# Performance work log

Measured on AMD Instinct MI355X. Metric: run time of the kernel, lower is better.

## Reference

```python
import jax, jax.numpy as jnp
import numpy as np

B, S, C, P, M, H = 64, 512, 862, 96, 512, 128  # batch, seq_len, enc_in, pred_len, mem_num, hid_size


def setup_inputs() -> dict:
    key = jax.random.key(0)
    ks = jax.random.split(key, 8)
    x = jax.random.normal(ks[0], (B, S, C), dtype=jnp.float32)
    # nn.Linear default init scale ~ 1/sqrt(fan_in)
    W1 = jax.random.normal(ks[1], (H, S), dtype=jnp.float32) / np.float32(np.sqrt(S))
    b1 = jnp.zeros((H,), dtype=jnp.float32)
    Wp = jax.random.normal(ks[2], (H, H), dtype=jnp.float32) / np.float32(np.sqrt(H))
    bp = jnp.zeros((H,), dtype=jnp.float32)
    W2 = jax.random.normal(ks[3], (P, 2 * H), dtype=jnp.float32) / np.float32(np.sqrt(2 * H))
    b2 = jnp.zeros((P,), dtype=jnp.float32)
    # xavier_normal_ with relu gain: std = sqrt(2) * sqrt(2/(fan_in+fan_out))
    mem_std = np.float32(np.sqrt(2.0) * np.sqrt(2.0 / (M + H)))
    memory = jax.random.normal(ks[4], (M, H), dtype=jnp.float32) * mem_std
    return dict(x=x, W1=W1, b1=b1, Wp=Wp, bp=bp, W2=W2, b2=b2, memory=memory)


def reference(x, W1, b1, Wp, bp, W2, b2, memory):
    b, s, c = x.shape
    # get_repre: Linear1 over seq dim, sigmoid, projector
    r = jax.nn.sigmoid(jnp.einsum('bsc,hs->bch', x, W1) + b1)   # [B, C, H]
    r = jnp.einsum('bch,gh->bcg', r, Wp) + bp                    # [B, C, H]
    r = r.reshape(-1, H)                                         # [N, H], N = B*C
    # memory_enhance: codebook attention (topk/distance loss does not affect output)
    att = jax.nn.softmax(jnp.einsum('nd,fd->nf', r, memory), axis=1)  # [N, M]
    out = jnp.einsum('nf,fd->nd', att, memory)                        # [N, H]
    rep = jnp.concatenate([out, r], axis=1).reshape(b, c, 2 * H)      # [B, C, 2H]
    # predict: Linear2 then permute to [B, pred_len, C]
    res = jnp.einsum('bcd,pd->bcp', rep, W2) + b2
    return jnp.transpose(res, (0, 2, 1))
```

## Files before the change

kernel.cpp:

```cpp
#include <hip/hip_runtime.h>
#include <hip/hip_bf16.h>

typedef __attribute__((ext_vector_type(4))) float f32x4;
typedef __attribute__((ext_vector_type(8))) short s16x8;

#define DEVI __device__ __forceinline__

constexpr int S = 512, C = 862, P = 96, H = 128, BATCH = 64;

DEVI short f2bf(float f) {
  unsigned u = __builtin_bit_cast(unsigned, f);
  u += 0x7fffu + ((u >> 16) & 1u);
  return (short)(u >> 16);
}

DEVI unsigned pk2(float a, float b) {
  return (unsigned)(unsigned short)f2bf(a) | ((unsigned)(unsigned short)f2bf(b) << 16);
}

DEVI s16x8 mk8(const float* v) {
  s16x8 r;
#pragma unroll
  for (int i = 0; i < 8; ++i) r[i] = f2bf(v[i]);
  return r;
}

DEVI void gload16(const void* g, void* l) {
  __builtin_amdgcn_global_load_lds(
      (const __attribute__((address_space(1))) void*)g,
      (__attribute__((address_space(3))) void*)l, 16, 0, 0);
}

template <int NK>
DEVI void redistN(const unsigned* p01, const unsigned* p23, int sA, int hi,
                  s16x8* f) {
#pragma unroll
  for (int kc = 0; kc < NK; ++kc) {
    unsigned a0 = __shfl(p01[2 * kc], sA),      b0 = __shfl(p01[2 * kc + 1], sA);
    unsigned a1 = __shfl(p23[2 * kc], sA),      b1 = __shfl(p23[2 * kc + 1], sA);
    unsigned a2 = __shfl(p01[2 * kc], sA + 16), b2 = __shfl(p01[2 * kc + 1], sA + 16);
    unsigned a3 = __shfl(p23[2 * kc], sA + 16), b3 = __shfl(p23[2 * kc + 1], sA + 16);
    union { s16x8 v; unsigned u[4]; } t;
    t.u[0] = hi ? b0 : a0;
    t.u[1] = hi ? b1 : a1;
    t.u[2] = hi ? b2 : a2;
    t.u[3] = hi ? b3 : a3;
    f[kc] = t.v;
  }
}

__global__ __launch_bounds__(256) void k0_convert(
    const float* __restrict__ W1, const float* __restrict__ Wp,
    const float* __restrict__ W2, const float* __restrict__ mem,
    short* __restrict__ W1b, short* __restrict__ WpS, short* __restrict__ W2b,
    short* __restrict__ membS, short* __restrict__ memTS) {
  int i = blockIdx.x * 256 + threadIdx.x;
  if (i < 65536) { W1b[i] = f2bf(W1[i]); return; }
  i -= 65536;
  if (i < 16384) {
    int g = i >> 7, h = i & 127;
    WpS[(g << 7) + (h ^ ((g & 7) << 3))] = f2bf(Wp[i]);
    return;
  }
  i -= 16384;
  if (i < 24576) { W2b[i] = f2bf(W2[i]); return; }
  i -= 24576;
  if (i < 65536) {
    int f = i >> 7, d = i & 127;
    short v = f2bf(mem[i]);
    membS[((f >> 6) << 13) + ((f & 63) << 7) + (d ^ ((f & 7) << 3))] = v;
    memTS[((f >> 6) << 13) + (d << 6) + ((f & 63) ^ ((d & 7) << 3))] = v;
  }
}

__global__ __launch_bounds__(512, 4) void k1_repre(
    const float* __restrict__ x, const short* __restrict__ W1b,
    const float* __restrict__ b1, short* __restrict__ R1b) {
  __shared__ short xt[2][64 * 64];
  __shared__ short w1t[2][128 * 64];
  const int b = blockIdx.y;
  const int c0 = blockIdx.x * 64;
  const int tid = threadIdx.x;
  const int l = tid & 63, w = tid >> 6;
  const int l15 = l & 15, l4 = l >> 4;
  const int csub = (w >> 2) * 32, hsub = (w & 3) * 32;

  f32x4 acc[2][2];
#pragma unroll
  for (int ct = 0; ct < 2; ++ct)
#pragma unroll
    for (int ht = 0; ht < 2; ++ht) acc[ct][ht] = (f32x4){0.f, 0.f, 0.f, 0.f};

  const int cme = tid & 63;
  const int oct = tid >> 6;
  const bool cv = (c0 + cme) < C;
  const float* xsrc0 = x + (size_t)b * S * C + c0 + cme;
  const int hh = tid >> 2, qq = tid & 3;

  float xv[8];
  s16x8 wv[2];
  {
    const float* src = xsrc0 + (size_t)(oct * 8) * C;
#pragma unroll
    for (int i = 0; i < 8; ++i) xv[i] = cv ? src[(size_t)i * C] : 0.f;
    const short* wsrc = W1b + hh * 512;
    wv[0] = *(const s16x8*)&wsrc[qq * 8];
    wv[1] = *(const s16x8*)&wsrc[(qq + 4) * 8];
  }

  for (int kt = 0; kt < 8; ++kt) {
    const int pb = kt & 1;
    *(s16x8*)&xt[pb][cme * 64 + (oct ^ (cme & 7)) * 8] = mk8(xv);
    *(s16x8*)&w1t[pb][hh * 64 + (qq ^ (hh & 7)) * 8] = wv[0];
    *(s16x8*)&w1t[pb][hh * 64 + ((qq + 4) ^ (hh & 7)) * 8] = wv[1];
    __syncthreads();
    if (kt < 7) {
      int kn = kt + 1;
      const float* src = xsrc0 + (size_t)(kn * 64 + oct * 8) * C;
#pragma unroll
      for (int i = 0; i < 8; ++i) xv[i] = cv ? src[(size_t)i * C] : 0.f;
      const short* wsrc = W1b + hh * 512 + kn * 64;
      wv[0] = *(const s16x8*)&wsrc[qq * 8];
      wv[1] = *(const s16x8*)&wsrc[(qq + 4) * 8];
    }
    s16x8 af[2][2], bf[2][2];
#pragma unroll
    for (int ct = 0; ct < 2; ++ct)
#pragma unroll
      for (int kc = 0; kc < 2; ++kc) {
        int row = csub + ct * 16 + l15;
        int slot = kc * 4 + l4;
        af[ct][kc] = *(const s16x8*)&xt[pb][row * 64 + (slot ^ (row & 7)) * 8];
      }
#pragma unroll
    for (int ht = 0; ht < 2; ++ht)
#pragma unroll
      for (int kc = 0; kc < 2; ++kc) {
        int row = hsub + ht * 16 + l15;
        int slot = kc * 4 + l4;
        bf[ht][kc] = *(const s16x8*)&w1t[pb][row * 64 + (slot ^ (row & 7)) * 8];
      }
#pragma unroll
    for (int ct = 0; ct < 2; ++ct)
#pragma unroll
      for (int ht = 0; ht < 2; ++ht)
#pragma unroll
        for (int kc = 0; kc < 2; ++kc)
          acc[ct][ht] = __builtin_amdgcn_mfma_f32_16x16x32_bf16(
              af[ct][kc], bf[ht][kc], acc[ct][ht], 0, 0, 0);
  }
#pragma unroll
  for (int ct = 0; ct < 2; ++ct) {
#pragma unroll
    for (int ht = 0; ht < 2; ++ht) {
      int hcol = hsub + ht * 16 + l15;
      float bias = b1[hcol];
#pragma unroll
      for (int e = 0; e < 4; ++e) {
        int crow = csub + ct * 16 + l4 * 4 + e;
        if (c0 + crow < C) {
          float v = acc[ct][ht][e] + bias;
          float sg = 1.f / (1.f + __expf(-v));
          R1b[((size_t)b * C + c0 + crow) * 128 + hcol] = f2bf(sg);
        }
      }
    }
  }
}

__global__ __launch_bounds__(512, 2) void k2_fused(
    const short* __restrict__ R1b, const short* __restrict__ WpS,
    const float* __restrict__ bp, const short* __restrict__ membS,
    const short* __restrict__ memTS, const short* __restrict__ W2b,
    const float* __restrict__ b2, float* __restrict__ out) {
  __shared__ __align__(16) char lds[65536];
  float* resf = (float*)lds;

  const int b = blockIdx.y, c0 = blockIdx.x * 128;
  const int valid = (C - c0 < 128) ? (C - c0) : 128;
  const int tid = threadIdx.x, l = tid & 63, w = tid >> 6;
  const int l15 = l & 15, l4 = l >> 4;
  const int sA = l15 + 32 * (l4 & 1);
  const int hi = (l4 >> 1) & 1;
  const int xr = (l15 & 7) << 4;
  const int cb = l4 * 16;
  const size_t n0 = (size_t)b * C + c0;

  const int rloc = 16 * w + l15;
  const int rr = rloc < valid ? rloc : valid - 1;

  {
    const char* gwp = (const char*)WpS;
    const char* gmb = (const char*)membS;
    const char* gmt = (const char*)memTS;
#pragma unroll
    for (int i = 0; i < 4; ++i) {
      int o = (w * 4 + i) * 1024;
      gload16(gwp + o + l * 16, lds + 32768 + o);
    }
#pragma unroll
    for (int i = 0; i < 2; ++i) {
      int o = (w * 2 + i) * 1024;
      gload16(gmb + o + l * 16, lds + o);
      gload16(gmt + o + l * 16, lds + 16384 + o);
    }
  }

  s16x8 rb[4];
  {
    const short* r1row = R1b + (n0 + rr) * 128;
#pragma unroll
    for (int kc = 0; kc < 4; ++kc)
      rb[kc] = *(const s16x8*)&r1row[kc * 32 + l4 * 8];
  }
  __syncthreads();

  unsigned rpk01[8], rpk23[8];
  {
    const char* bufWp = lds + 32768;
#pragma unroll
    for (int gt = 0; gt < 8; ++gt) {
      f32x4 acc = (f32x4){0.f, 0.f, 0.f, 0.f};
#pragma unroll
      for (int kc = 0; kc < 4; ++kc) {
        s16x8 af = *(const s16x8*)(bufWp + (gt * 16 + l15) * 256 + ((kc * 64 + cb) ^ xr));
        acc = __builtin_amdgcn_mfma_f32_16x16x32_bf16(af, rb[kc], acc, 0, 0, 0);
      }
      f32x4 bq = *(const f32x4*)&bp[gt * 16 + l4 * 4];
      rpk01[gt] = pk2(acc[0] + bq[0], acc[1] + bq[1]);
      rpk23[gt] = pk2(acc[2] + bq[2], acc[3] + bq[3]);
    }
  }
  s16x8 r2f[4];
  redistN<4>(rpk01, rpk23, sA, hi, r2f);
  __syncthreads();

  float m_run = -1e30f, s_run = 0.f;
  f32x4 oacc[8];
#pragma unroll
  for (int dt = 0; dt < 8; ++dt) oacc[dt] = (f32x4){0.f, 0.f, 0.f, 0.f};

  for (int s = 0; s < 8; ++s) {
    char* bufp = lds + ((s & 1) << 15);
    if (s < 7) {
      char* bufn = lds + (((s + 1) & 1) << 15);
      const char* gmb = (const char*)membS + (size_t)(s + 1) * 16384;
      const char* gmt = (const char*)memTS + (size_t)(s + 1) * 16384;
#pragma unroll
      for (int i = 0; i < 2; ++i) {
        int o = (w * 2 + i) * 1024;
        gload16(gmb + o + l * 16, bufn + o);
        gload16(gmt + o + l * 16, bufn + 16384 + o);
      }
    }
    f32x4 lg[4];
#pragma unroll
    for (int ft = 0; ft < 4; ++ft) {
      lg[ft] = (f32x4){0.f, 0.f, 0.f, 0.f};
#pragma unroll
      for (int kc = 0; kc < 4; ++kc) {
        s16x8 af = *(const s16x8*)(bufp + (ft * 16 + l15) * 256 + ((kc * 64 + cb) ^ xr));
        lg[ft] = __builtin_amdgcn_mfma_f32_16x16x32_bf16(af, r2f[kc], lg[ft], 0, 0, 0);
      }
    }
    float mx = lg[0][0];
#pragma unroll
    for (int ft = 0; ft < 4; ++ft)
#pragma unroll
      for (int e = 0; e < 4; ++e) mx = fmaxf(mx, lg[ft][e]);
    mx = fmaxf(mx, __shfl_xor(mx, 16));
    mx = fmaxf(mx, __shfl_xor(mx, 32));
    float mn = fmaxf(m_run, mx);
    float sc = __expf(m_run - mn);
    float ps = 0.f;
#pragma unroll
    for (int ft = 0; ft < 4; ++ft)
#pragma unroll
      for (int e = 0; e < 4; ++e) {
        float p = __expf(lg[ft][e] - mn);
        lg[ft][e] = p;
        ps += p;
      }
    ps += __shfl_xor(ps, 16);
    ps += __shfl_xor(ps, 32);
    s_run = s_run * sc + ps;
    m_run = mn;
#pragma unroll
    for (int dt = 0; dt < 8; ++dt)
#pragma unroll
      for (int e = 0; e < 4; ++e) oacc[dt][e] *= sc;
    unsigned ppk01[4], ppk23[4];
#pragma unroll
    for (int ft = 0; ft < 4; ++ft) {
      ppk01[ft] = pk2(lg[ft][0], lg[ft][1]);
      ppk23[ft] = pk2(lg[ft][2], lg[ft][3]);
    }
    s16x8 pf[2];
    redistN<2>(ppk01, ppk23, sA, hi, pf);
#pragma unroll
    for (int dt = 0; dt < 8; ++dt) {
#pragma unroll
      for (int kc = 0; kc < 2; ++kc) {
        s16x8 af = *(const s16x8*)(bufp + 16384 + (dt * 16 + l15) * 128 + ((kc * 64 + cb) ^ xr));
        oacc[dt] = __builtin_amdgcn_mfma_f32_16x16x32_bf16(af, pf[kc], oacc[dt], 0, 0, 0);
      }
    }
    __syncthreads();
  }

  s16x8 of[4];
  {
    float inv = 1.f / s_run;
    unsigned opk01[8], opk23[8];
#pragma unroll
    for (int dt = 0; dt < 8; ++dt) {
      opk01[dt] = pk2(oacc[dt][0] * inv, oacc[dt][1] * inv);
      opk23[dt] = pk2(oacc[dt][2] * inv, oacc[dt][3] * inv);
    }
    redistN<4>(opk01, opk23, sA, hi, of);
  }

#pragma unroll
  for (int pt = 0; pt < 6; ++pt) {
    f32x4 acc = (f32x4){0.f, 0.f, 0.f, 0.f};
#pragma unroll
    for (int kc = 0; kc < 4; ++kc) {
      s16x8 af = *(const s16x8*)&W2b[(pt * 16 + l15) * 256 + kc * 32 + l4 * 8];
      acc = __builtin_amdgcn_mfma_f32_16x16x32_bf16(af, of[kc], acc, 0, 0, 0);
    }
#pragma unroll
    for (int kc = 0; kc < 4; ++kc) {
      s16x8 af = *(const s16x8*)&W2b[(pt * 16 + l15) * 256 + 128 + kc * 32 + l4 * 8];
      acc = __builtin_amdgcn_mfma_f32_16x16x32_bf16(af, r2f[kc], acc, 0, 0, 0);
    }
    f32x4 bq = *(const f32x4*)&b2[pt * 16 + l4 * 4];
#pragma unroll
    for (int e = 0; e < 4; ++e)
      resf[rloc * 97 + pt * 16 + l4 * 4 + e] = acc[e] + bq[e];
  }
  __syncthreads();
  {
    int c = tid & 127, p0 = tid >> 7;
    if (c < valid) {
      float* dst = out + (size_t)b * P * C + c0 + c;
#pragma unroll
      for (int j = 0; j < 24; ++j) {
        int p = p0 + j * 4;
        dst[(size_t)p * C] = resf[c * 97 + p];
      }
    }
  }
}

extern "C" void kernel_launch(void* const* d_in, const int* in_sizes, int n_in,
                              void* d_out, int out_size, void* d_ws, size_t ws_size,
                              hipStream_t stream) {
  const float* x   = (const float*)d_in[0];
  const float* W1  = (const float*)d_in[1];
  const float* b1  = (const float*)d_in[2];
  const float* Wp  = (const float*)d_in[3];
  const float* bpv = (const float*)d_in[4];
  const float* W2  = (const float*)d_in[5];
  const float* b2  = (const float*)d_in[6];
  const float* mem = (const float*)d_in[7];
  char* ws = (char*)d_ws;
  short* W1b   = (short*)(ws);
  short* WpS   = (short*)(ws + 131072);
  short* W2b   = (short*)(ws + 163840);
  short* membS = (short*)(ws + 212992);
  short* memTS = (short*)(ws + 344064);
  short* R1b   = (short*)(ws + 475136);
  float* outp = (float*)d_out;

  k0_convert<<<672, 256, 0, stream>>>(W1, Wp, W2, mem, W1b, WpS, W2b, membS, memTS);
  dim3 grid1(14, BATCH);
  k1_repre<<<grid1, 512, 0, stream>>>(x, W1b, b1, R1b);
  dim3 grid2(7, BATCH);
  k2_fused<<<grid2, 512, 0, stream>>>(R1b, WpS, bpv, membS, memTS, W2b, b2, outp);
}
```

Before: 95.24 us.

## Rewrite k1 GEMM to load operands straight to registers without LDS staging

The first-stage kernel no longer stages x and W1 tiles through double-buffered shared memory with barriers. Each wave now owns 32 channels across all 128 hidden units, reads W1 fragments and strided x values from global memory directly into MFMA operands, and writes packed bf16 sigmoid outputs. The aim is to remove LDS traffic and __syncthreads overhead. In exchange, W1 is reloaded from global/L2 by every wave, the x reads are 4-byte strided loads with less coalescing, and the grid shrinks to 256-thread blocks.

```diff
diff --git a/kernel.cpp b/kernel.cpp
--- a/kernel.cpp
+++ b/kernel.cpp
@@ -73,96 +73,65 @@
   }
 }
 
-__global__ __launch_bounds__(512, 4) void k1_repre(
+__global__ __launch_bounds__(256, 2) void k1_repre(
     const float* __restrict__ x, const short* __restrict__ W1b,
     const float* __restrict__ b1, short* __restrict__ R1b) {
-  __shared__ short xt[2][64 * 64];
-  __shared__ short w1t[2][128 * 64];
   const int b = blockIdx.y;
-  const int c0 = blockIdx.x * 64;
-  const int tid = threadIdx.x;
-  const int l = tid & 63, w = tid >> 6;
+  const int tid = threadIdx.x, l = tid & 63, w = tid >> 6;
   const int l15 = l & 15, l4 = l >> 4;
-  const int csub = (w >> 2) * 32, hsub = (w & 3) * 32;
-
-  f32x4 acc[2][2];
-#pragma unroll
-  for (int ct = 0; ct < 2; ++ct)
-#pragma unroll
-    for (int ht = 0; ht < 2; ++ht) acc[ct][ht] = (f32x4){0.f, 0.f, 0.f, 0.f};
-
-  const int cme = tid & 63;
-  const int oct = tid >> 6;
-  const bool cv = (c0 + cme) < C;
-  const float* xsrc0 = x + (size_t)b * S * C + c0 + cme;
-  const int hh = tid >> 2, qq = tid & 3;
-
-  float xv[8];
-  s16x8 wv[2];
-  {
-    const float* src = xsrc0 + (size_t)(oct * 8) * C;
-#pragma unroll
-    for (int i = 0; i < 8; ++i) xv[i] = cv ? src[(size_t)i * C] : 0.f;
-    const short* wsrc = W1b + hh * 512;
-    wv[0] = *(const s16x8*)&wsrc[qq * 8];
-    wv[1] = *(const s16x8*)&wsrc[(qq + 4) * 8];
-  }
-
-  for (int kt = 0; kt < 8; ++kt) {
-    const int pb = kt & 1;
-    *(s16x8*)&xt[pb][cme * 64 + (oct ^ (cme & 7)) * 8] = mk8(xv);
-    *(s16x8*)&w1t[pb][hh * 64 + (qq ^ (hh & 7)) * 8] = wv[0];
-    *(s16x8*)&w1t[pb][hh * 64 + ((qq + 4) ^ (hh & 7)) * 8] = wv[1];
-    __syncthreads();
-    if (kt < 7) {
-      int kn = kt + 1;
-      const float* src = xsrc0 + (size_t)(kn * 64 + oct * 8) * C;
-#pragma unroll
-      for (int i = 0; i < 8; ++i) xv[i] = cv ? src[(size_t)i * C] : 0.f;
-      const short* wsrc = W1b + hh * 512 + kn * 64;
-      wv[0] = *(const s16x8*)&wsrc[qq * 8];
-      wv[1] = *(const s16x8*)&wsrc[(qq + 4) * 8];
-    }
-    s16x8 af[2][2], bf[2][2];
-#pragma unroll
-    for (int ct = 0; ct < 2; ++ct)
-#pragma unroll
-      for (int kc = 0; kc < 2; ++kc) {
-        int row = csub + ct * 16 + l15;
-        int slot = kc * 4 + l4;
-        af[ct][kc] = *(const s16x8*)&xt[pb][row * 64 + (slot ^ (row & 7)) * 8];
-      }
-#pragma unroll
-    for (int ht = 0; ht < 2; ++ht)
-#pragma unroll
-      for (int kc = 0; kc < 2; ++kc) {
-        int row = hsub + ht * 16 + l15;
-        int slot = kc * 4 + l4;
-        bf[ht][kc] = *(const s16x8*)&w1t[pb][row * 64 + (slot ^ (row & 7)) * 8];
-      }
-#pragma unroll
-    for (int ct = 0; ct < 2; ++ct)
-#pragma unroll
-      for (int ht = 0; ht < 2; ++ht)
-#pragma unroll
-        for (int kc = 0; kc < 2; ++kc)
-          acc[ct][ht] = __builtin_amdgcn_mfma_f32_16x16x32_bf16(
-              af[ct][kc], bf[ht][kc], acc[ct][ht], 0, 0, 0);
-  }
-#pragma unroll
-  for (int ct = 0; ct < 2; ++ct) {
-#pragma unroll
-    for (int ht = 0; ht < 2; ++ht) {
-      int hcol = hsub + ht * 16 + l15;
-      float bias = b1[hcol];
-#pragma unroll
-      for (int e = 0; e < 4; ++e) {
-        int crow = csub + ct * 16 + l4 * 4 + e;
-        if (c0 + crow < C) {
-          float v = acc[ct][ht][e] + bias;
-          float sg = 1.f / (1.f + __expf(-v));
-          R1b[((size_t)b * C + c0 + crow) * 128 + hcol] = f2bf(sg);
-        }
+  const int cw0 = blockIdx.x * 128 + w * 32;
+  if (cw0 >= C) return;
+  const float* xb = x + (size_t)b * S * C;
+
+  f32x4 acc[2][8];
+#pragma unroll
+  for (int g = 0; g < 2; ++g)
+#pragma unroll
+    for (int t = 0; t < 8; ++t) acc[g][t] = (f32x4){0.f, 0.f, 0.f, 0.f};
+
+  int cc[2];
+#pragma unroll
+  for (int g = 0; g < 2; ++g) {
+    int c = cw0 + g * 16 + l15;
+    cc[g] = c < C ? c : C - 1;
+  }
+
+#pragma unroll 4
+  for (int kc = 0; kc < 16; ++kc) {
+    s16x8 af[8];
+#pragma unroll
+    for (int t = 0; t < 8; ++t)
+      af[t] = *(const s16x8*)&W1b[(t * 16 + l15) * 512 + kc * 32 + l4 * 8];
+#pragma unroll
+    for (int g = 0; g < 2; ++g) {
+      const float* src = xb + (size_t)(kc * 32 + l4 * 8) * C + cc[g];
+      float v[8];
+#pragma unroll
+      for (int i = 0; i < 8; ++i) v[i] = src[(size_t)i * C];
+      s16x8 bx = mk8(v);
+#pragma unroll
+      for (int t = 0; t < 8; ++t)
+        acc[g][t] = __builtin_amdgcn_mfma_f32_16x16x32_bf16(af[t], bx, acc[g][t], 0, 0, 0);
+    }
+  }
+
+#pragma unroll
+  for (int g = 0; g < 2; ++g) {
+    int c = cw0 + g * 16 + l15;
+    if (c < C) {
+      short* dst = R1b + ((size_t)b * C + c) * 128;
+#pragma unroll
+      for (int t = 0; t < 8; ++t) {
+        int h0 = t * 16 + l4 * 4;
+        f32x4 bq = *(const f32x4*)&b1[h0];
+        float s0 = 1.f / (1.f + __expf(-(acc[g][t][0] + bq[0])));
+        float s1 = 1.f / (1.f + __expf(-(acc[g][t][1] + bq[1])));
+        float s2 = 1.f / (1.f + __expf(-(acc[g][t][2] + bq[2])));
+        float s3 = 1.f / (1.f + __expf(-(acc[g][t][3] + bq[3])));
+        uint2 pp;
+        pp.x = pk2(s0, s1);
+        pp.y = pk2(s2, s3);
+        *(uint2*)&dst[h0] = pp;
       }
     }
   }
@@ -373,8 +342,8 @@
   float* outp = (float*)d_out;
 
   k0_convert<<<672, 256, 0, stream>>>(W1, Wp, W2, mem, W1b, WpS, W2b, membS, memTS);
-  dim3 grid1(14, BATCH);
-  k1_repre<<<grid1, 512, 0, stream>>>(x, W1b, b1, R1b);
+  dim3 grid1(7, BATCH);
+  k1_repre<<<grid1, 256, 0, stream>>>(x, W1b, b1, R1b);
   dim3 grid2(7, BATCH);
   k2_fused<<<grid2, 512, 0, stream>>>(R1b, WpS, bpv, membS, memTS, W2b, b2, outp);
 }
```

New measurement: 113.3 us. 1.19x slower.

## Fuse Linear1+sigmoid GEMM into the memory-attention kernel, dropping R1 round trip

Applied to the files above, without the earlier changes.

Merges the first-stage GEMM over the sequence dimension into the second kernel. Each block computes its 128 channels of sigmoid(xW1+b1) in registers and redistributes them straight into MFMA operand layout, so the bf16 R1 intermediate is no longer written to and re-read from global memory and one launch disappears. In exchange, the fused kernel runs with fewer blocks (7x64 at occupancy 2 instead of 14x64 at 4), and its LDS is reused between phases, which lowers parallelism for the memory-bound x read.

```diff
diff --git a/kernel.cpp b/kernel.cpp
--- a/kernel.cpp
+++ b/kernel.cpp
@@ -73,107 +73,17 @@
   }
 }
 
-__global__ __launch_bounds__(512, 4) void k1_repre(
+__global__ __launch_bounds__(512, 2) void k12_fused(
     const float* __restrict__ x, const short* __restrict__ W1b,
-    const float* __restrict__ b1, short* __restrict__ R1b) {
-  __shared__ short xt[2][64 * 64];
-  __shared__ short w1t[2][128 * 64];
-  const int b = blockIdx.y;
-  const int c0 = blockIdx.x * 64;
-  const int tid = threadIdx.x;
-  const int l = tid & 63, w = tid >> 6;
-  const int l15 = l & 15, l4 = l >> 4;
-  const int csub = (w >> 2) * 32, hsub = (w & 3) * 32;
-
-  f32x4 acc[2][2];
-#pragma unroll
-  for (int ct = 0; ct < 2; ++ct)
-#pragma unroll
-    for (int ht = 0; ht < 2; ++ht) acc[ct][ht] = (f32x4){0.f, 0.f, 0.f, 0.f};
-
-  const int cme = tid & 63;
-  const int oct = tid >> 6;
-  const bool cv = (c0 + cme) < C;
-  const float* xsrc0 = x + (size_t)b * S * C + c0 + cme;
-  const int hh = tid >> 2, qq = tid & 3;
-
-  float xv[8];
-  s16x8 wv[2];
-  {
-    const float* src = xsrc0 + (size_t)(oct * 8) * C;
-#pragma unroll
-    for (int i = 0; i < 8; ++i) xv[i] = cv ? src[(size_t)i * C] : 0.f;
-    const short* wsrc = W1b + hh * 512;
-    wv[0] = *(const s16x8*)&wsrc[qq * 8];
-    wv[1] = *(const s16x8*)&wsrc[(qq + 4) * 8];
-  }
-
-  for (int kt = 0; kt < 8; ++kt) {
-    const int pb = kt & 1;
-    *(s16x8*)&xt[pb][cme * 64 + (oct ^ (cme & 7)) * 8] = mk8(xv);
-    *(s16x8*)&w1t[pb][hh * 64 + (qq ^ (hh & 7)) * 8] = wv[0];
-    *(s16x8*)&w1t[pb][hh * 64 + ((qq + 4) ^ (hh & 7)) * 8] = wv[1];
-    __syncthreads();
-    if (kt < 7) {
-      int kn = kt + 1;
-      const float* src = xsrc0 + (size_t)(kn * 64 + oct * 8) * C;
-#pragma unroll
-      for (int i = 0; i < 8; ++i) xv[i] = cv ? src[(size_t)i * C] : 0.f;
-      const short* wsrc = W1b + hh * 512 + kn * 64;
-      wv[0] = *(const s16x8*)&wsrc[qq * 8];
-      wv[1] = *(const s16x8*)&wsrc[(qq + 4) * 8];
-    }
-    s16x8 af[2][2], bf[2][2];
-#pragma unroll
-    for (int ct = 0; ct < 2; ++ct)
-#pragma unroll
-      for (int kc = 0; kc < 2; ++kc) {
-        int row = csub + ct * 16 + l15;
-        int slot = kc * 4 + l4;
-        af[ct][kc] = *(const s16x8*)&xt[pb][row * 64 + (slot ^ (row & 7)) * 8];
-      }
-#pragma unroll
-    for (int ht = 0; ht < 2; ++ht)
-#pragma unroll
-      for (int kc = 0; kc < 2; ++kc) {
-        int row = hsub + ht * 16 + l15;
-        int slot = kc * 4 + l4;
-        bf[ht][kc] = *(const s16x8*)&w1t[pb][row * 64 + (slot ^ (row & 7)) * 8];
-      }
-#pragma unroll
-    for (int ct = 0; ct < 2; ++ct)
-#pragma unroll
-      for (int ht = 0; ht < 2; ++ht)
-#pragma unroll
-        for (int kc = 0; kc < 2; ++kc)
-          acc[ct][ht] = __builtin_amdgcn_mfma_f32_16x16x32_bf16(
-              af[ct][kc], bf[ht][kc], acc[ct][ht], 0, 0, 0);
-  }
-#pragma unroll
-  for (int ct = 0; ct < 2; ++ct) {
-#pragma unroll
-    for (int ht = 0; ht < 2; ++ht) {
-      int hcol = hsub + ht * 16 + l15;
-      float bias = b1[hcol];
-#pragma unroll
-      for (int e = 0; e < 4; ++e) {
-        int crow = csub + ct * 16 + l4 * 4 + e;
-        if (c0 + crow < C) {
-          float v = acc[ct][ht][e] + bias;
-          float sg = 1.f / (1.f + __expf(-v));
-          R1b[((size_t)b * C + c0 + crow) * 128 + hcol] = f2bf(sg);
-        }
-      }
-    }
-  }
-}
-
-__global__ __launch_bounds__(512, 2) void k2_fused(
-    const short* __restrict__ R1b, const short* __restrict__ WpS,
+    const float* __restrict__ b1, const short* __restrict__ WpS,
     const float* __restrict__ bp, const short* __restrict__ membS,
     const short* __restrict__ memTS, const short* __restrict__ W2b,
     const float* __restrict__ b2, float* __restrict__ out) {
   __shared__ __align__(16) char lds[65536];
+  short* xt0 = (short*)(lds);
+  short* xt1 = (short*)(lds + 16384);
+  short* w1t0 = (short*)(lds + 32768);
+  short* w1t1 = (short*)(lds + 49152);
   float* resf = (float*)lds;
 
   const int b = blockIdx.y, c0 = blockIdx.x * 128;
@@ -184,10 +94,82 @@
   const int hi = (l4 >> 1) & 1;
   const int xr = (l15 & 7) << 4;
   const int cb = l4 * 16;
-  const size_t n0 = (size_t)b * C + c0;
-
   const int rloc = 16 * w + l15;
-  const int rr = rloc < valid ? rloc : valid - 1;
+
+  s16x8 rb[4];
+  {
+    const int cme = tid & 127, o2 = tid >> 7;
+    const bool cv = (c0 + cme) < C;
+    const float* xsrc0 = x + (size_t)b * S * C + c0 + cme;
+    const int hh = tid >> 2, qq = tid & 3;
+
+    f32x4 acc[8];
+#pragma unroll
+    for (int t = 0; t < 8; ++t) acc[t] = (f32x4){0.f, 0.f, 0.f, 0.f};
+
+    float xv[2][8];
+    s16x8 wv[2];
+    {
+#pragma unroll
+      for (int j = 0; j < 2; ++j) {
+        const float* src = xsrc0 + (size_t)((o2 + j * 4) * 8) * C;
+#pragma unroll
+        for (int i = 0; i < 8; ++i) xv[j][i] = cv ? src[(size_t)i * C] : 0.f;
+      }
+      const short* wsrc = W1b + hh * 512;
+      wv[0] = *(const s16x8*)&wsrc[qq * 8];
+      wv[1] = *(const s16x8*)&wsrc[(qq + 4) * 8];
+    }
+
+    for (int kt = 0; kt < 8; ++kt) {
+      short* xt = (kt & 1) ? xt1 : xt0;
+      short* w1t = (kt & 1) ? w1t1 : w1t0;
+#pragma unroll
+      for (int j = 0; j < 2; ++j)
+        *(s16x8*)&xt[cme * 64 + ((o2 + j * 4) ^ (cme & 7)) * 8] = mk8(xv[j]);
+      *(s16x8*)&w1t[hh * 64 + (qq ^ (hh & 7)) * 8] = wv[0];
+      *(s16x8*)&w1t[hh * 64 + ((qq + 4) ^ (hh & 7)) * 8] = wv[1];
+      __syncthreads();
+      if (kt < 7) {
+        int kn = kt + 1;
+#pragma unroll
+        for (int j = 0; j < 2; ++j) {
+          const float* src = xsrc0 + (size_t)(kn * 64 + (o2 + j * 4) * 8) * C;
+#pragma unroll
+          for (int i = 0; i < 8; ++i) xv[j][i] = cv ? src[(size_t)i * C] : 0.f;
+        }
+        const short* wsrc = W1b + hh * 512 + kn * 64;
+        wv[0] = *(const s16x8*)&wsrc[qq * 8];
+        wv[1] = *(const s16x8*)&wsrc[(qq + 4) * 8];
+      }
+      s16x8 bx[2];
+#pragma unroll
+      for (int kc = 0; kc < 2; ++kc)
+        bx[kc] = *(const s16x8*)&xt[rloc * 64 + ((kc * 4 + l4) ^ (l15 & 7)) * 8];
+#pragma unroll
+      for (int t = 0; t < 8; ++t) {
+#pragma unroll
+        for (int kc = 0; kc < 2; ++kc) {
+          s16x8 af = *(const s16x8*)&w1t[(t * 16 + l15) * 64 + ((kc * 4 + l4) ^ (l15 & 7)) * 8];
+          acc[t] = __builtin_amdgcn_mfma_f32_16x16x32_bf16(af, bx[kc], acc[t], 0, 0, 0);
+        }
+      }
+      if (kt == 7) __syncthreads();
+    }
+
+    unsigned p01[8], p23[8];
+#pragma unroll
+    for (int t = 0; t < 8; ++t) {
+      f32x4 bq = *(const f32x4*)&b1[t * 16 + l4 * 4];
+      float s0 = 1.f / (1.f + __expf(-(acc[t][0] + bq[0])));
+      float s1 = 1.f / (1.f + __expf(-(acc[t][1] + bq[1])));
+      float s2 = 1.f / (1.f + __expf(-(acc[t][2] + bq[2])));
+      float s3 = 1.f / (1.f + __expf(-(acc[t][3] + bq[3])));
+      p01[t] = pk2(s0, s1);
+      p23[t] = pk2(s2, s3);
+    }
+    redistN<4>(p01, p23, sA, hi, rb);
+  }
 
   {
     const char* gwp = (const char*)WpS;
@@ -204,14 +186,6 @@
       gload16(gmb + o + l * 16, lds + o);
       gload16(gmt + o + l * 16, lds + 16384 + o);
     }
-  }
-
-  s16x8 rb[4];
-  {
-    const short* r1row = R1b + (n0 + rr) * 128;
-#pragma unroll
-    for (int kc = 0; kc < 4; ++kc)
-      rb[kc] = *(const s16x8*)&r1row[kc * 32 + l4 * 8];
   }
   __syncthreads();
 
@@ -369,12 +343,9 @@
   short* W2b   = (short*)(ws + 163840);
   short* membS = (short*)(ws + 212992);
   short* memTS = (short*)(ws + 344064);
-  short* R1b   = (short*)(ws + 475136);
   float* outp = (float*)d_out;
 
   k0_convert<<<672, 256, 0, stream>>>(W1, Wp, W2, mem, W1b, WpS, W2b, membS, memTS);
-  dim3 grid1(14, BATCH);
-  k1_repre<<<grid1, 512, 0, stream>>>(x, W1b, b1, R1b);
-  dim3 grid2(7, BATCH);
-  k2_fused<<<grid2, 512, 0, stream>>>(R1b, WpS, bpv, membS, memTS, W2b, b2, outp);
-}
+  dim3 grid(7, BATCH);
+  k12_fused<<<grid, 512, 0, stream>>>(x, W1b, b1, WpS, bpv, membS, memTS, W2b, b2, outp);
+}
```

Result: faster. 83.85 us (-12.0%).
